# Optimization experiments

Hardware: AMD Instinct MI355X
Metric: run time of the kernel (lower is better)

The kernel has to match this reference:

```python
import jax, jax.numpy as jnp
import numpy as np

L, B, H, R = 128, 4, 768, 24
LN_EPS = 1e-5


def setup_inputs() -> dict:
    key = jax.random.key(0)
    ks = jax.random.split(key, 10)
    s = 1.0 / np.sqrt(H)
    return {
        "h_re": jax.random.normal(ks[0], (L, B, H), jnp.float32),
        "h_share": jax.random.normal(ks[1], (L, B, H), jnp.float32),
        "mask": jnp.ones((L, B), jnp.float32),
        # r: Linear(2H -> H)
        "r_w": jax.random.normal(ks[2], (H, 2 * H), jnp.float32) * s,
        "r_b": jnp.zeros((H,), jnp.float32),
        # hid2hid: Linear(3H -> H)
        "hid_w": jax.random.normal(ks[3], (H, 3 * H), jnp.float32) * s,
        "hid_b": jnp.zeros((H,), jnp.float32),
        # LayerNorm(H)
        "ln_g": jnp.ones((H,), jnp.float32),
        "ln_b": jnp.zeros((H,), jnp.float32),
        # hid2rel: Linear(H -> R)
        "rel_w": jax.random.normal(ks[4], (R, H), jnp.float32) * s,
        "rel_b": jnp.zeros((R,), jnp.float32),
    }


def reference(h_re, h_share, mask, r_w, r_b, hid_w, hid_b, ln_g, ln_b, rel_w, rel_b):
    # h_global = max_over_length( tanh( Linear([h_share; h_re]) ) )  -> [B, H]
    # Decompose concat-linear into two additive projections (same math).
    w_sh, w_re = r_w[:, :H], r_w[:, H:]
    g = jnp.tanh(jnp.einsum('lbh,kh->lbk', h_share, w_sh)
                 + jnp.einsum('lbh,kh->lbk', h_re, w_re) + r_b)
    g = jnp.max(g, axis=0)  # [B, H]

    # hid2hid(cat(r1, r2, g)) = h_re@W1^T (bcast over j) + h_re@W2^T (bcast over i) + g@W3^T + b
    w1, w2, w3 = hid_w[:, :H], hid_w[:, H:2 * H], hid_w[:, 2 * H:]
    p1 = jnp.einsum('lbh,kh->lbk', h_re, w1)        # [L, B, H] -> varies with i
    p2 = jnp.einsum('lbh,kh->lbk', h_re, w2)        # [L, B, H] -> varies with j
    pg = jnp.einsum('bh,kh->bk', g, w3) + hid_b     # [B, H]
    z = p1[:, None, :, :] + p2[None, :, :, :] + pg  # [L, L, B, H]

    # LayerNorm over last dim
    mu = jnp.mean(z, axis=-1, keepdims=True)
    var = jnp.mean(jnp.square(z - mu), axis=-1, keepdims=True)
    z = (z - mu) * jax.lax.rsqrt(var + LN_EPS) * ln_g + ln_b

    # ELU (dropout = identity in eval), then sigmoid(hid2rel)
    z = jax.nn.elu(z)
    re = jax.nn.sigmoid(jnp.einsum('ijbh,rh->ijbr', z, rel_w) + rel_b)  # [L, L, B, R]

    # pairwise mask: mask[i,b] * mask[j,b]
    m = mask[:, None, :] * mask[None, :, :]        # [L, L, B]
    return re * m[..., None]
```

## Files before the change

kernel.cpp:

```cpp
#include <hip/hip_runtime.h>
#include <hip/hip_bf16.h>
#include <math.h>

#define L 128
#define B 4
#define H 768
#define LN_EPS 1e-5f
#define XROWS 272
#define DSTRIDE 73984

typedef __attribute__((ext_vector_type(8))) short short8;
typedef __attribute__((ext_vector_type(4))) float f32x4;
typedef __attribute__((ext_vector_type(16))) float f32x16;

static __device__ __forceinline__ unsigned f2bfu(float f) {
    unsigned u = __float_as_uint(f);
    return (u + 0x7FFFu + ((u >> 16) & 1u)) >> 16;
}
static __device__ __forceinline__ uint2 pk4(float4 v) {
    uint2 o;
    o.x = f2bfu(v.x) | (f2bfu(v.y) << 16);
    o.y = f2bfu(v.z) | (f2bfu(v.w) << 16);
    return o;
}
static __device__ __forceinline__ unsigned short f2b(float f) {
    union { __hip_bfloat16 h; unsigned short u; } cv;
    cv.h = __float2bfloat16(f);
    return cv.u;
}
static __device__ __forceinline__ float4 unpk4(uint2 p) {
    return make_float4(__uint_as_float(p.x << 16),
                       __uint_as_float(p.x & 0xffff0000u),
                       __uint_as_float(p.y << 16),
                       __uint_as_float(p.y & 0xffff0000u));
}
static __device__ __forceinline__ unsigned fkey(float x) {
    unsigned u = __float_as_uint(x);
    return (u >> 31) ? ~u : (u | 0x80000000u);
}

__global__ __launch_bounds__(256) void kConv(const float* __restrict__ h_re,
                                             const float* __restrict__ h_share,
                                             const float* __restrict__ r_w,
                                             const float* __restrict__ hid_w,
                                             const float* __restrict__ rel_w,
                                             unsigned short* __restrict__ apack,
                                             unsigned short* __restrict__ wpackA,
                                             unsigned short* __restrict__ wpackB,
                                             unsigned short* __restrict__ rwb2,
                                             unsigned int* __restrict__ gmax) {
    int t = blockIdx.x * 256 + threadIdx.x;
    if (t >= 397056) return;
    if (t < 98304) {
        int m = t / 192, oct = t % 192, k = oct * 8;
        const float* src = (k < 768) ? (h_share + (size_t)m * 768 + k)
                                     : (h_re + (size_t)m * 768 + k - 768);
        float4 x = *(const float4*)src, y = *(const float4*)(src + 4);
        int mt = m >> 4, lr = m & 15, ks = k >> 5, lq = (k >> 3) & 3;
        uint2* dst = (uint2*)(apack + (((size_t)mt * 48 + ks) * 64 + lq * 16 + lr) * 8);
        dst[0] = pk4(x); dst[1] = pk4(y);
    } else if (t < 245760) {
        int t2 = t - 98304;
        int n = t2 / 192, oct = t2 % 192, k = oct * 8;
        const float* src = r_w + (size_t)n * 1536 + k;
        float4 x = *(const float4*)src, y = *(const float4*)(src + 4);
        int nt = n >> 4, lr = n & 15, ks = k >> 5, lq = (k >> 3) & 3;
        uint2* dst = (uint2*)(wpackA + (((size_t)nt * 48 + ks) * 64 + lq * 16 + lr) * 8);
        dst[0] = pk4(x); dst[1] = pk4(y);
    } else if (t < 393216) {
        int t3 = t - 245760;
        int n = t3 / 96, oct = t3 % 96, k = oct * 8;
        int half = (n >= 768) ? 1 : 0;
        const float* src = hid_w + (size_t)(n - half * 768) * 2304 + half * 768 + k;
        float4 x = *(const float4*)src, y = *(const float4*)(src + 4);
        int nt = n >> 4, lr = n & 15, ks = k >> 5, lq = (k >> 3) & 3;
        uint2* dst = (uint2*)(wpackB + (((size_t)nt * 24 + ks) * 64 + lq * 16 + lr) * 8);
        dst[0] = pk4(x); dst[1] = pk4(y);
    } else if (t < 396288) {
        int t4 = t - 393216;
        int s = t4 >> 6, l = t4 & 63;
        int row = l & 31;
        uint2 o0 = make_uint2(0u, 0u), o1 = o0;
        if (row < 24) {
            const float* src = rel_w + (size_t)row * 768 + s * 16 + (l >> 5) * 8;
            o0 = pk4(*(const float4*)src);
            o1 = pk4(*(const float4*)(src + 4));
        }
        uint2* dst = (uint2*)(rwb2 + (size_t)t4 * 8);
        dst[0] = o0; dst[1] = o1;
    } else {
        int t6 = t - 396288;
        gmax[t6] = 0u;
        gmax[768 + t6] = 0u;
        gmax[1536 + t6] = 0u;
        gmax[2304 + t6] = 0u;
    }
}

template<int KSW>
static __device__ __forceinline__ void gemm_steps(const unsigned short* __restrict__ a0p,
                                                  const unsigned short* __restrict__ a1p,
                                                  const unsigned short* __restrict__ w0p,
                                                  const unsigned short* __restrict__ w1p,
                                                  f32x4 acc[2][2]) {
#pragma unroll
    for (int s = 0; s < KSW; s++) {
        short8 a0 = *(const short8*)(a0p + (size_t)s * 512);
        short8 a1 = *(const short8*)(a1p + (size_t)s * 512);
        short8 w0 = *(const short8*)(w0p + (size_t)s * 512);
        short8 w1 = *(const short8*)(w1p + (size_t)s * 512);
        acc[0][0] = __builtin_amdgcn_mfma_f32_16x16x32_bf16(a0, w0, acc[0][0], 0, 0, 0);
        acc[0][1] = __builtin_amdgcn_mfma_f32_16x16x32_bf16(a0, w1, acc[0][1], 0, 0, 0);
        acc[1][0] = __builtin_amdgcn_mfma_f32_16x16x32_bf16(a1, w0, acc[1][0], 0, 0, 0);
        acc[1][1] = __builtin_amdgcn_mfma_f32_16x16x32_bf16(a1, w1, acc[1][1], 0, 0, 0);
    }
}

__global__ __launch_bounds__(256) void kGemm(const unsigned short* __restrict__ apack,
                                             const unsigned short* __restrict__ wpackA,
                                             const unsigned short* __restrict__ wpackB,
                                             unsigned int* __restrict__ gmax,
                                             unsigned short* __restrict__ xb16) {
    __shared__ float red[4][4][64][4];
    int id = blockIdx.x;
    int tid = threadIdx.x, lane = tid & 63, wv = tid >> 6;
    int lq = lane >> 4, lr = lane & 15;
    bool isA = id < 384;
    f32x4 acc[2][2] = {{{0.f,0.f,0.f,0.f},{0.f,0.f,0.f,0.f}},
                       {{0.f,0.f,0.f,0.f},{0.f,0.f,0.f,0.f}}};
    int mt0, nt0;
    if (isA) {
        mt0 = (id / 24) * 2; nt0 = (id % 24) * 2;
        const unsigned short* a0p = apack + ((size_t)mt0 * 48 + wv * 12) * 512 + lane * 8;
        const unsigned short* w0p = wpackA + ((size_t)nt0 * 48 + wv * 12) * 512 + lane * 8;
        gemm_steps<12>(a0p, a0p + 48 * 512, w0p, w0p + 48 * 512, acc);
    } else {
        int id2 = id - 384;
        mt0 = (id2 / 48) * 2; nt0 = (id2 % 48) * 2;
        const unsigned short* a0p = apack + ((size_t)mt0 * 48 + 24 + wv * 6) * 512 + lane * 8;
        const unsigned short* w0p = wpackB + ((size_t)nt0 * 24 + wv * 6) * 512 + lane * 8;
        gemm_steps<6>(a0p, a0p + 48 * 512, w0p, w0p + 24 * 512, acc);
    }
#pragma unroll
    for (int mi = 0; mi < 2; mi++)
#pragma unroll
        for (int ni = 0; ni < 2; ni++)
            *(f32x4*)&red[wv][mi * 2 + ni][lane][0] = acc[mi][ni];
    __syncthreads();
    if (wv != 0) return;

    f32x4 s2[2][2];
#pragma unroll
    for (int mi = 0; mi < 2; mi++)
#pragma unroll
        for (int ni = 0; ni < 2; ni++) {
            f32x4 v = *(f32x4*)&red[0][mi * 2 + ni][lane][0];
#pragma unroll
            for (int w = 1; w < 4; w++) {
                f32x4 u = *(f32x4*)&red[w][mi * 2 + ni][lane][0];
                v[0] += u[0]; v[1] += u[1]; v[2] += u[2]; v[3] += u[3];
            }
            s2[mi][ni] = v;
        }

    if (isA) {
#pragma unroll
        for (int ni = 0; ni < 2; ni++)
#pragma unroll
            for (int q = 0; q < 4; q++) {
                float mx = fmaxf(s2[0][ni][q], s2[1][ni][q]);
                mx = fmaxf(mx, __shfl_xor(mx, 16, 64));
                mx = fmaxf(mx, __shfl_xor(mx, 32, 64));
                if (lq == 0) {
                    int n = (nt0 + ni) * 16 + lr;
                    atomicMax(&gmax[q * 768 + n], fkey(mx));
                }
            }
    } else {
#pragma unroll
        for (int mi = 0; mi < 2; mi++)
#pragma unroll
            for (int ni = 0; ni < 2; ni++)
#pragma unroll
                for (int q = 0; q < 4; q++) {
                    int m = (mt0 + mi) * 16 + lq * 4 + q;
                    int n = (nt0 + ni) * 16 + lr;
                    int b = m & 3, l = m >> 2;
                    size_t row = (n < 768) ? (size_t)l : (size_t)(128 + l);
                    int col = (n < 768) ? n : n - 768;
                    xb16[((size_t)b * XROWS + row) * 768 + col] = f2b(s2[mi][ni][q]);
                }
    }
}

__global__ __launch_bounds__(256) void kPgPack(const unsigned int* __restrict__ gmax,
                                               const float* __restrict__ r_b,
                                               const float* __restrict__ hid_w,
                                               const float* __restrict__ hid_b,
                                               unsigned short* xb16,
                                               unsigned short* __restrict__ xpack) {
    int blk = blockIdx.x, tid = threadIdx.x;
    if (blk >= 48) {
        int t = (blk - 48) * 256 + tid;
        int b = t / 24576, rem = t % 24576;
        int r = rem / 96, k8 = rem % 96;
        const uint2* src = (const uint2*)(xb16 + ((size_t)b * XROWS + r) * 768 + k8 * 8);
        uint2 v0 = src[0], v1 = src[1];
        size_t dst = ((((size_t)(b * 17 + (r >> 4)) * 24 + (k8 >> 2)) * 64)
                      + (k8 & 3) * 16 + (r & 15)) * 8;
        uint2* d = (uint2*)(xpack + dst);
        d[0] = v0; d[1] = v1;
        return;
    }
    __shared__ float sg[768];
    __shared__ float sp[4][64];
    __shared__ float spg[64];
    int kt = blk % 12, b = blk / 12;
    for (int v = tid; v < 768; v += 256) {
        unsigned key = gmax[b * 768 + v];
        unsigned bits = (key & 0x80000000u) ? (key & 0x7FFFFFFFu) : ~key;
        sg[v] = tanhf(__uint_as_float(bits) + r_b[v]);
    }
    __syncthreads();
    int kk = tid & 63, hc = tid >> 6;
    int k = kt * 64 + kk;
    const float4* w4 = (const float4*)hid_w;
    const float4* g4 = (const float4*)sg;
    float acc = 0.f;
    for (int h = hc * 48; h < hc * 48 + 48; h++) {
        float4 gv = g4[h];
        float4 wv = w4[(size_t)k * 576 + 384 + h];
        acc += gv.x * wv.x + gv.y * wv.y + gv.z * wv.z + gv.w * wv.w;
    }
    sp[hc][kk] = acc;
    __syncthreads();
    if (hc == 0) {
        float pgv = sp[0][kk] + sp[1][kk] + sp[2][kk] + sp[3][kk] + hid_b[k];
        spg[kk] = pgv;
        xb16[((size_t)b * XROWS + 256) * 768 + k] = f2b(pgv);
    }
    __syncthreads();
    if (tid < 128) {
        int ksl = tid >> 6, lane = tid & 63;
        int ks = kt * 2 + ksl;
        int row16 = lane & 15;
        int kbase = ksl * 32 + (lane >> 4) * 8;
        unsigned short vals[8];
        if (row16 == 0) {
#pragma unroll
            for (int e = 0; e < 8; e++) vals[e] = f2b(spg[kbase + e]);
        } else if (row16 == 1) {
#pragma unroll
            for (int e = 0; e < 8; e++) vals[e] = 0x3F80;
        } else {
#pragma unroll
            for (int e = 0; e < 8; e++) vals[e] = 0;
        }
        uint2* d = (uint2*)(xpack + (((size_t)(b * 17 + 16) * 24 + ks) * 64 + lane) * 8);
        d[0] = *(uint2*)&vals[0];
        d[1] = *(uint2*)&vals[4];
    }
}

__global__ __launch_bounds__(64) void kGram(const unsigned short* __restrict__ xpack,
                                            float* __restrict__ D) {
    int t = blockIdx.x, b = blockIdx.y;
    int it, jt;
    if (t < 64)      { it = t >> 3;  jt = 8 + (t & 7); }
    else if (t < 80) { it = t - 64;  jt = t - 64; }
    else             { it = t - 80;  jt = 16; }
    int lane = threadIdx.x, lq = lane >> 4, lr = lane & 15;
    const unsigned short* ar = xpack + ((size_t)(b * 17 + it) * 24 * 64 + lane) * 8;
    const unsigned short* wr = xpack + ((size_t)(b * 17 + jt) * 24 * 64 + lane) * 8;
    f32x4 acc = {0.f, 0.f, 0.f, 0.f};
#pragma unroll 8
    for (int s = 0; s < 24; s++) {
        short8 a = *(const short8*)(ar + (size_t)s * 512);
        short8 w = *(const short8*)(wr + (size_t)s * 512);
        acc = __builtin_amdgcn_mfma_f32_16x16x32_bf16(a, w, acc, 0, 0, 0);
    }
    float* Db = D + (size_t)b * DSTRIDE;
#pragma unroll
    for (int q = 0; q < 4; q++)
        Db[(size_t)(it * 16 + lq * 4 + q) * XROWS + jt * 16 + lr] = acc[q];
}

__global__ __launch_bounds__(512, 6) void kC(const unsigned short* __restrict__ xb16,
                                             const float* __restrict__ ln_g,
                                             const float* __restrict__ ln_b,
                                             const unsigned short* __restrict__ rwb2,
                                             const float* __restrict__ rel_b,
                                             const float* __restrict__ D,
                                             const float* __restrict__ mask,
                                             float* __restrict__ out) {
    __shared__ __align__(16) unsigned char smem[49920];
    __shared__ float smu[32], srs[32];
    unsigned short (*zls)[780] = (unsigned short (*)[780])smem;
    int i = blockIdx.x, b = blockIdx.y, j0 = blockIdx.z * 32;
    int tid = threadIdx.x, lane = tid & 63, wave = tid >> 6;

    if (tid < 32) {
        const float* Db = D + (size_t)b * DSTRIDE;
        int vr = 128 + j0 + tid;
        float Su1 = Db[(size_t)i * XROWS + 257];
        float Su2 = Db[(size_t)i * XROWS + i];
        float up  = Db[(size_t)i * XROWS + 256];
        float Sp1 = Db[(size_t)256 * XROWS + 257];
        float Sp2 = Db[(size_t)256 * XROWS + 256];
        float Sv1 = Db[(size_t)vr * XROWS + 257];
        float Sv2 = Db[(size_t)vr * XROWS + vr];
        float Dij = Db[(size_t)i * XROWS + vr];
        float cvj = Db[(size_t)vr * XROWS + 256];
        float s1 = Su1 + Sp1 + Sv1;
        float s2 = Su2 + Sp2 + Sv2 + 2.f * (Dij + up + cvj);
        float mu = s1 * (1.f / 768.f);
        smu[tid] = mu;
        srs[tid] = rsqrtf(s2 * (1.f / 768.f) - mu * mu + LN_EPS);
    }
    const uint2* ur = (const uint2*)(xb16 + ((size_t)b * XROWS + i) * 768);
    const uint2* pr = (const uint2*)(xb16 + ((size_t)b * XROWS + 256) * 768);
    const float4* lg4 = (const float4*)ln_g;
    const float4* lb4 = (const float4*)ln_b;
    float4 t1[3], gg[3], bb[3];
#pragma unroll
    for (int s = 0; s < 3; s++) {
        int c = lane + 64 * s;
        float4 x = unpk4(ur[c]), y = unpk4(pr[c]);
        t1[s] = make_float4(x.x + y.x, x.y + y.y, x.z + y.z, x.w + y.w);
        gg[s] = lg4[c];
        bb[s] = lb4[c];
    }
    __syncthreads();

#pragma unroll
    for (int jj = 0; jj < 4; jj++) {
        int j = wave * 4 + jj;
        float mu = smu[j], rs = srs[j];
        const uint2* vr2 = (const uint2*)(xb16 + ((size_t)b * XROWS + 128 + j0 + j) * 768);
        uint2* zrow = (uint2*)&zls[j][0];
#pragma unroll
        for (int s = 0; s < 3; s++) {
            int c = lane + 64 * s;
            float4 vv = unpk4(vr2[c]);
            float A0 = rs * gg[s].x, A1 = rs * gg[s].y, A2 = rs * gg[s].z, A3 = rs * gg[s].w;
            float C0 = fmaf(-mu, A0, bb[s].x), C1 = fmaf(-mu, A1, bb[s].y);
            float C2 = fmaf(-mu, A2, bb[s].z), C3 = fmaf(-mu, A3, bb[s].w);
            float z0 = fmaf(t1[s].x + vv.x, A0, C0);
            float z1 = fmaf(t1[s].y + vv.y, A1, C1);
            float z2 = fmaf(t1[s].z + vv.z, A2, C2);
            float z3 = fmaf(t1[s].w + vv.w, A3, C3);
            z0 = fmaxf(z0, __expf(fminf(z0, 0.f)) - 1.f);
            z1 = fmaxf(z1, __expf(fminf(z1, 0.f)) - 1.f);
            z2 = fmaxf(z2, __expf(fminf(z2, 0.f)) - 1.f);
            z3 = fmaxf(z3, __expf(fminf(z3, 0.f)) - 1.f);
            uint2 o;
            o.x = (unsigned)f2b(z0) | ((unsigned)f2b(z1) << 16);
            o.y = (unsigned)f2b(z2) | ((unsigned)f2b(z3) << 16);
            zrow[c] = o;
        }
    }
    __syncthreads();

    int arow = lane & 31, ahi = lane >> 5;
    f32x16 acc = {0.f,0.f,0.f,0.f, 0.f,0.f,0.f,0.f, 0.f,0.f,0.f,0.f, 0.f,0.f,0.f,0.f};
    const unsigned short* bptr = rwb2 + ((size_t)(wave * 6) * 64 + lane) * 8;
#pragma unroll
    for (int st = 0; st < 6; st++) {
        int s = wave * 6 + st;
        short8 a  = *(const short8*)&zls[arow][s * 16 + ahi * 8];
        short8 bf = *(const short8*)(bptr + (size_t)st * 512);
        acc = __builtin_amdgcn_mfma_f32_32x32x16_bf16(a, bf, acc, 0, 0, 0);
    }
    __syncthreads();
    float* pf = (float*)smem;
#pragma unroll
    for (int r = 0; r < 16; r++) {
        int row = (r & 3) + 8 * (r >> 2) + 4 * ahi;
        pf[wave * 1024 + row * 32 + arow] = acc[r];
    }
    __syncthreads();

#pragma unroll
    for (int e0 = 0; e0 < 2; e0++) {
        int e = tid + e0 * 512;
        int row = e >> 5, col = e & 31;
        if (col < 24) {
            float v = 0.f;
#pragma unroll
            for (int w = 0; w < 8; w++) v += pf[w * 1024 + e];
            int jgl = j0 + row;
            float mval = mask[i * 4 + b] * mask[jgl * 4 + b];
            out[((size_t)(i * 128 + jgl) * 4 + b) * 24 + col] =
                mval / (1.f + __expf(-(v + rel_b[col])));
        }
    }
}

extern "C" void kernel_launch(void* const* d_in, const int* in_sizes, int n_in,
                              void* d_out, int out_size, void* d_ws, size_t ws_size,
                              hipStream_t stream) {
    const float* h_re    = (const float*)d_in[0];
    const float* h_share = (const float*)d_in[1];
    const float* mask    = (const float*)d_in[2];
    const float* r_w     = (const float*)d_in[3];
    const float* r_b     = (const float*)d_in[4];
    const float* hid_w   = (const float*)d_in[5];
    const float* hid_b   = (const float*)d_in[6];
    const float* ln_g    = (const float*)d_in[7];
    const float* ln_b    = (const float*)d_in[8];
    const float* rel_w   = (const float*)d_in[9];
    const float* rel_b   = (const float*)d_in[10];
    float* out = (float*)d_out;

    float* ws = (float*)d_ws;
    unsigned short* apack  = (unsigned short*)(ws);
    unsigned short* wpackA = (unsigned short*)(ws + 393216);
    unsigned short* wpackB = (unsigned short*)(ws + 983040);
    unsigned short* xb16   = (unsigned short*)(ws + 1572864);
    float*          D      = ws + 1990656;
    unsigned int*   gmax   = (unsigned int*)(ws + 2286592);
    unsigned short* rwb2   = (unsigned short*)(ws + 2289664);
    unsigned short* xpack  = (unsigned short*)(ws);

    kConv<<<1552, 256, 0, stream>>>(h_re, h_share, r_w, hid_w, rel_w,
                                    apack, wpackA, wpackB, rwb2, gmax);
    kGemm<<<1152, 256, 0, stream>>>(apack, wpackA, wpackB, gmax, xb16);
    kPgPack<<<432, 256, 0, stream>>>(gmax, r_b, hid_w, hid_b, xb16, xpack);
    kGram<<<dim3(97, 4), 64, 0, stream>>>(xpack, D);
    kC<<<dim3(L, B, 4), 512, 0, stream>>>(xb16, ln_g, ln_b, rwb2, rel_b,
                                          D, mask, out);
}
```

Measured before the change: 65.89 us.

## Compute LayerNorm statistics in-register via wave reductions instead of Gram-matrix precompute

Drops the packing pass and the Gram-matrix MFMA kernel that precomputed per-(i,j) LayerNorm mean and variance from row dot products. Each wave in kC now builds z for its row, sums it and its squares, and reduces both with xor shuffles to get mu and rstd. This removes one kernel launch, the pack copy and the D workspace round trip. In exchange every (i,j,b) row pays a 64-lane butterfly reduction and keeps z in registers, which raises register pressure in the main kernel.

```diff
diff --git a/kernel.cpp b/kernel.cpp
--- a/kernel.cpp
+++ b/kernel.cpp
@@ -7,7 +7,6 @@
 #define H 768
 #define LN_EPS 1e-5f
 #define XROWS 272
-#define DSTRIDE 73984
 
 typedef __attribute__((ext_vector_type(8))) short short8;
 typedef __attribute__((ext_vector_type(4))) float f32x4;
@@ -193,29 +192,14 @@
     }
 }
 
-__global__ __launch_bounds__(256) void kPgPack(const unsigned int* __restrict__ gmax,
-                                               const float* __restrict__ r_b,
-                                               const float* __restrict__ hid_w,
-                                               const float* __restrict__ hid_b,
-                                               unsigned short* xb16,
-                                               unsigned short* __restrict__ xpack) {
-    int blk = blockIdx.x, tid = threadIdx.x;
-    if (blk >= 48) {
-        int t = (blk - 48) * 256 + tid;
-        int b = t / 24576, rem = t % 24576;
-        int r = rem / 96, k8 = rem % 96;
-        const uint2* src = (const uint2*)(xb16 + ((size_t)b * XROWS + r) * 768 + k8 * 8);
-        uint2 v0 = src[0], v1 = src[1];
-        size_t dst = ((((size_t)(b * 17 + (r >> 4)) * 24 + (k8 >> 2)) * 64)
-                      + (k8 & 3) * 16 + (r & 15)) * 8;
-        uint2* d = (uint2*)(xpack + dst);
-        d[0] = v0; d[1] = v1;
-        return;
-    }
+__global__ __launch_bounds__(256) void kPg(const unsigned int* __restrict__ gmax,
+                                           const float* __restrict__ r_b,
+                                           const float* __restrict__ hid_w,
+                                           const float* __restrict__ hid_b,
+                                           unsigned short* __restrict__ xb16) {
     __shared__ float sg[768];
     __shared__ float sp[4][64];
-    __shared__ float spg[64];
-    int kt = blk % 12, b = blk / 12;
+    int kt = blockIdx.x, b = blockIdx.y, tid = threadIdx.x;
     for (int v = tid; v < 768; v += 256) {
         unsigned key = gmax[b * 768 + v];
         unsigned bits = (key & 0x80000000u) ? (key & 0x7FFFFFFFu) : ~key;
@@ -236,53 +220,8 @@
     __syncthreads();
     if (hc == 0) {
         float pgv = sp[0][kk] + sp[1][kk] + sp[2][kk] + sp[3][kk] + hid_b[k];
-        spg[kk] = pgv;
         xb16[((size_t)b * XROWS + 256) * 768 + k] = f2b(pgv);
     }
-    __syncthreads();
-    if (tid < 128) {
-        int ksl = tid >> 6, lane = tid & 63;
-        int ks = kt * 2 + ksl;
-        int row16 = lane & 15;
-        int kbase = ksl * 32 + (lane >> 4) * 8;
-        unsigned short vals[8];
-        if (row16 == 0) {
-#pragma unroll
-            for (int e = 0; e < 8; e++) vals[e] = f2b(spg[kbase + e]);
-        } else if (row16 == 1) {
-#pragma unroll
-            for (int e = 0; e < 8; e++) vals[e] = 0x3F80;
-        } else {
-#pragma unroll
-            for (int e = 0; e < 8; e++) vals[e] = 0;
-        }
-        uint2* d = (uint2*)(xpack + (((size_t)(b * 17 + 16) * 24 + ks) * 64 + lane) * 8);
-        d[0] = *(uint2*)&vals[0];
-        d[1] = *(uint2*)&vals[4];
-    }
-}
-
-__global__ __launch_bounds__(64) void kGram(const unsigned short* __restrict__ xpack,
-                                            float* __restrict__ D) {
-    int t = blockIdx.x, b = blockIdx.y;
-    int it, jt;
-    if (t < 64)      { it = t >> 3;  jt = 8 + (t & 7); }
-    else if (t < 80) { it = t - 64;  jt = t - 64; }
-    else             { it = t - 80;  jt = 16; }
-    int lane = threadIdx.x, lq = lane >> 4, lr = lane & 15;
-    const unsigned short* ar = xpack + ((size_t)(b * 17 + it) * 24 * 64 + lane) * 8;
-    const unsigned short* wr = xpack + ((size_t)(b * 17 + jt) * 24 * 64 + lane) * 8;
-    f32x4 acc = {0.f, 0.f, 0.f, 0.f};
-#pragma unroll 8
-    for (int s = 0; s < 24; s++) {
-        short8 a = *(const short8*)(ar + (size_t)s * 512);
-        short8 w = *(const short8*)(wr + (size_t)s * 512);
-        acc = __builtin_amdgcn_mfma_f32_16x16x32_bf16(a, w, acc, 0, 0, 0);
-    }
-    float* Db = D + (size_t)b * DSTRIDE;
-#pragma unroll
-    for (int q = 0; q < 4; q++)
-        Db[(size_t)(it * 16 + lq * 4 + q) * XROWS + jt * 16 + lr] = acc[q];
 }
 
 __global__ __launch_bounds__(512, 6) void kC(const unsigned short* __restrict__ xb16,
@@ -290,33 +229,13 @@
                                              const float* __restrict__ ln_b,
                                              const unsigned short* __restrict__ rwb2,
                                              const float* __restrict__ rel_b,
-                                             const float* __restrict__ D,
                                              const float* __restrict__ mask,
                                              float* __restrict__ out) {
     __shared__ __align__(16) unsigned char smem[49920];
-    __shared__ float smu[32], srs[32];
     unsigned short (*zls)[780] = (unsigned short (*)[780])smem;
     int i = blockIdx.x, b = blockIdx.y, j0 = blockIdx.z * 32;
     int tid = threadIdx.x, lane = tid & 63, wave = tid >> 6;
 
-    if (tid < 32) {
-        const float* Db = D + (size_t)b * DSTRIDE;
-        int vr = 128 + j0 + tid;
-        float Su1 = Db[(size_t)i * XROWS + 257];
-        float Su2 = Db[(size_t)i * XROWS + i];
-        float up  = Db[(size_t)i * XROWS + 256];
-        float Sp1 = Db[(size_t)256 * XROWS + 257];
-        float Sp2 = Db[(size_t)256 * XROWS + 256];
-        float Sv1 = Db[(size_t)vr * XROWS + 257];
-        float Sv2 = Db[(size_t)vr * XROWS + vr];
-        float Dij = Db[(size_t)i * XROWS + vr];
-        float cvj = Db[(size_t)vr * XROWS + 256];
-        float s1 = Su1 + Sp1 + Sv1;
-        float s2 = Su2 + Sp2 + Sv2 + 2.f * (Dij + up + cvj);
-        float mu = s1 * (1.f / 768.f);
-        smu[tid] = mu;
-        srs[tid] = rsqrtf(s2 * (1.f / 768.f) - mu * mu + LN_EPS);
-    }
     const uint2* ur = (const uint2*)(xb16 + ((size_t)b * XROWS + i) * 768);
     const uint2* pr = (const uint2*)(xb16 + ((size_t)b * XROWS + 256) * 768);
     const float4* lg4 = (const float4*)ln_g;
@@ -330,25 +249,38 @@
         gg[s] = lg4[c];
         bb[s] = lb4[c];
     }
-    __syncthreads();
 
 #pragma unroll
     for (int jj = 0; jj < 4; jj++) {
         int j = wave * 4 + jj;
-        float mu = smu[j], rs = srs[j];
         const uint2* vr2 = (const uint2*)(xb16 + ((size_t)b * XROWS + 128 + j0 + j) * 768);
+        float4 z[3];
+        float s1 = 0.f, s2 = 0.f;
+#pragma unroll
+        for (int s = 0; s < 3; s++) {
+            float4 vv = unpk4(vr2[lane + 64 * s]);
+            vv.x += t1[s].x; vv.y += t1[s].y; vv.z += t1[s].z; vv.w += t1[s].w;
+            z[s] = vv;
+            s1 += vv.x + vv.y + vv.z + vv.w;
+            s2 += vv.x * vv.x + vv.y * vv.y + vv.z * vv.z + vv.w * vv.w;
+        }
+#pragma unroll
+        for (int off = 32; off > 0; off >>= 1) {
+            s1 += __shfl_xor(s1, off, 64);
+            s2 += __shfl_xor(s2, off, 64);
+        }
+        float mu = s1 * (1.f / 768.f);
+        float rs = rsqrtf(s2 * (1.f / 768.f) - mu * mu + LN_EPS);
         uint2* zrow = (uint2*)&zls[j][0];
 #pragma unroll
         for (int s = 0; s < 3; s++) {
-            int c = lane + 64 * s;
-            float4 vv = unpk4(vr2[c]);
             float A0 = rs * gg[s].x, A1 = rs * gg[s].y, A2 = rs * gg[s].z, A3 = rs * gg[s].w;
             float C0 = fmaf(-mu, A0, bb[s].x), C1 = fmaf(-mu, A1, bb[s].y);
             float C2 = fmaf(-mu, A2, bb[s].z), C3 = fmaf(-mu, A3, bb[s].w);
-            float z0 = fmaf(t1[s].x + vv.x, A0, C0);
-            float z1 = fmaf(t1[s].y + vv.y, A1, C1);
-            float z2 = fmaf(t1[s].z + vv.z, A2, C2);
-            float z3 = fmaf(t1[s].w + vv.w, A3, C3);
+            float z0 = fmaf(z[s].x, A0, C0);
+            float z1 = fmaf(z[s].y, A1, C1);
+            float z2 = fmaf(z[s].z, A2, C2);
+            float z3 = fmaf(z[s].w, A3, C3);
             z0 = fmaxf(z0, __expf(fminf(z0, 0.f)) - 1.f);
             z1 = fmaxf(z1, __expf(fminf(z1, 0.f)) - 1.f);
             z2 = fmaxf(z2, __expf(fminf(z2, 0.f)) - 1.f);
@@ -356,7 +288,7 @@
             uint2 o;
             o.x = (unsigned)f2b(z0) | ((unsigned)f2b(z1) << 16);
             o.y = (unsigned)f2b(z2) | ((unsigned)f2b(z3) << 16);
-            zrow[c] = o;
+            zrow[lane + 64 * s] = o;
         }
     }
     __syncthreads();
@@ -417,16 +349,13 @@
     unsigned short* wpackA = (unsigned short*)(ws + 393216);
     unsigned short* wpackB = (unsigned short*)(ws + 983040);
     unsigned short* xb16   = (unsigned short*)(ws + 1572864);
-    float*          D      = ws + 1990656;
-    unsigned int*   gmax   = (unsigned int*)(ws + 2286592);
-    unsigned short* rwb2   = (unsigned short*)(ws + 2289664);
-    unsigned short* xpack  = (unsigned short*)(ws);
+    unsigned int*   gmax   = (unsigned int*)(ws + 1990656);
+    unsigned short* rwb2   = (unsigned short*)(ws + 1993728);
 
     kConv<<<1552, 256, 0, stream>>>(h_re, h_share, r_w, hid_w, rel_w,
                                     apack, wpackA, wpackB, rwb2, gmax);
     kGemm<<<1152, 256, 0, stream>>>(apack, wpackA, wpackB, gmax, xb16);
-    kPgPack<<<432, 256, 0, stream>>>(gmax, r_b, hid_w, hid_b, xb16, xpack);
-    kGram<<<dim3(97, 4), 64, 0, stream>>>(xpack, D);
+    kPg<<<dim3(12, 4), 256, 0, stream>>>(gmax, r_b, hid_w, hid_b, xb16);
     kC<<<dim3(L, B, 4), 512, 0, stream>>>(xb16, ln_g, ln_b, rwb2, rel_b,
-                                          D, mask, out);
-}
+                                          mask, out);
+}
```

Measured after the change: 75.85 us. 15.1% more time.
